# Optimization experiments

Hardware: AMD Instinct MI355X
Metric: run time of the kernel (lower is better)

The kernel has to match this reference:

```python
import jax, jax.numpy as jnp
import numpy as np

D_IN = 1024
D_OUT = 1024
N_HEADS = 16
HEAD_DIM = D_OUT // N_HEADS


def setup_inputs() -> dict:
    key = jax.random.key(0)
    ks = jax.random.split(key, 5)
    scale = 0.02
    x = jax.random.normal(ks[0], (2, 2048, D_IN), dtype=jnp.float32)
    Wq = jax.random.normal(ks[1], (D_IN, D_OUT), dtype=jnp.float32) * scale
    Wk = jax.random.normal(ks[2], (D_IN, D_OUT), dtype=jnp.float32) * scale
    Wv = jax.random.normal(ks[3], (D_IN, D_OUT), dtype=jnp.float32) * scale
    Wout = jax.random.normal(ks[4], (D_OUT, D_OUT), dtype=jnp.float32) * scale
    return {"x": x, "Wq": Wq, "Wk": Wk, "Wv": Wv, "Wout": Wout}


def reference(x, Wq, Wk, Wv, Wout):
    batch, seq_len, _ = x.shape
    # projections (no bias)
    Q = (x @ Wq).reshape(batch, seq_len, N_HEADS, HEAD_DIM)
    K = (x @ Wk).reshape(batch, seq_len, N_HEADS, HEAD_DIM)
    V = (x @ Wv).reshape(batch, seq_len, N_HEADS, HEAD_DIM)
    # scores: [batch, heads, seq, seq]
    scores = jnp.einsum("bqhd,bkhd->bhqk", Q, K) / jnp.sqrt(
        jnp.asarray(HEAD_DIM, dtype=x.dtype)
    )
    # causal mask: positions k > q masked to -inf
    causal = jnp.tril(jnp.ones((seq_len, seq_len), dtype=bool))
    scores = jnp.where(causal[None, None], scores, -jnp.inf)
    weights = jax.nn.softmax(scores, axis=-1)
    vectors = jnp.einsum("bhqk,bkhd->bqhd", weights, V)
    vectors = vectors.reshape(batch, seq_len, D_OUT)
    return vectors @ Wout
```

## Files before the change

### kernel.cpp

```cpp
#include <hip/hip_runtime.h>
#include <hip/hip_bf16.h>


typedef __attribute__((ext_vector_type(8))) _Float16 vhalf8;
typedef __attribute__((ext_vector_type(4))) _Float16 vhalf4;
typedef __attribute__((ext_vector_type(4))) float vfloat4;

#define D_MODEL 1024
#define SEQ     2048
#define NB      2
#define NH      16
#define HD      64

#define SCALE_K1 0.18033688f

__device__ __forceinline__ void async16(const void* g, void* l) {
  __builtin_amdgcn_global_load_lds(
      (const __attribute__((address_space(1))) unsigned int*)g,
      (__attribute__((address_space(3))) unsigned int*)l, 16, 0, 0);
}

__global__ __launch_bounds__(256) void prep(
    const float* __restrict__ x,
    const float* __restrict__ Wq, const float* __restrict__ Wk,
    const float* __restrict__ Wv, const float* __restrict__ Wo,
    _Float16* __restrict__ Xh, _Float16* __restrict__ Wt_qkv,
    _Float16* __restrict__ Wot) {
  int z = blockIdx.z;
  int t = threadIdx.x;
  if (z == 4) {
    int id = blockIdx.y * 16 + blockIdx.x;
#pragma unroll
    for (int pass = 0; pass < 8; pass++) {
      size_t i = ((size_t)(pass * 256 + id) * 256 + t) * 8;
      float4 a = *(const float4*)&x[i];
      float4 b = *(const float4*)&x[i + 4];
      vhalf8 h;
      h[0] = (_Float16)a.x; h[1] = (_Float16)a.y;
      h[2] = (_Float16)a.z; h[3] = (_Float16)a.w;
      h[4] = (_Float16)b.x; h[5] = (_Float16)b.y;
      h[6] = (_Float16)b.z; h[7] = (_Float16)b.w;
      *(vhalf8*)&Xh[i] = h;
    }
    return;
  }
  __shared__ _Float16 tile[64][65];
  const float* in = (z == 0) ? Wq : (z == 1) ? Wk : (z == 2) ? Wv : Wo;
  _Float16* out = (z < 3) ? (Wt_qkv + (size_t)z * 1024 * 1024) : Wot;
  int c0 = blockIdx.x * 64, r0 = blockIdx.y * 64;
  int tc = t & 63, tr = t >> 6;
#pragma unroll
  for (int p = 0; p < 16; p++) {
    int r = tr + p * 4;
    tile[r][tc] = (_Float16)in[(size_t)(r0 + r) * 1024 + c0 + tc];
  }
  __syncthreads();
#pragma unroll
  for (int p = 0; p < 16; p++) {
    int r = tr + p * 4;
    out[(size_t)(c0 + r) * 1024 + r0 + tc] = tile[tc][r];
  }
}

template <int BN>
__global__ __launch_bounds__(256) void gemm128(
    const _Float16* __restrict__ A, const _Float16* __restrict__ Bt,
    _Float16* __restrict__ Ch, float* __restrict__ Cf,
    _Float16* __restrict__ Vt, int M, int N, int K, int mode) {
  constexpr int ACH = 8;
  constexpr int BCH = BN / 16;
  constexpr int CPW = (ACH + BCH) / 4;
  constexpr int JN = BN / 32;
  __shared__ _Float16 As[128 * 32];
  __shared__ _Float16 Bs[BN * 32];
  int m0 = blockIdx.x * 128, n0 = blockIdx.y * BN;
  int t = threadIdx.x;
  int lane = t & 63, wave = t >> 6;
  int wm = (wave >> 1) * 64, wn = (wave & 1) * (BN / 2);
  int col = lane & 15, quad = lane >> 4;
  int srow = lane >> 2;
  int gcol = (((lane & 3) ^ (srow & 3)) << 3);

  vfloat4 acc[4][JN];
#pragma unroll
  for (int i = 0; i < 4; i++)
#pragma unroll
    for (int j = 0; j < JN; j++) {
      acc[i][j][0] = 0.f; acc[i][j][1] = 0.f;
      acc[i][j][2] = 0.f; acc[i][j][3] = 0.f;
    }

  int xq = (quad ^ (col & 3)) * 8;

  for (int k0 = 0; k0 < K; k0 += 32) {
    __syncthreads();
#pragma unroll
    for (int j = 0; j < CPW; j++) {
      int c = wave * CPW + j;
      if (c < ACH) {
        int row = c * 16 + srow;
        async16(&A[(size_t)(m0 + row) * K + k0 + gcol], &As[c * 512]);
      } else {
        int row = (c - ACH) * 16 + srow;
        async16(&Bt[(size_t)(n0 + row) * K + k0 + gcol], &Bs[(c - ACH) * 512]);
      }
    }
    __syncthreads();

    vhalf8 af[4], bf[JN];
#pragma unroll
    for (int i = 0; i < 4; i++)
      af[i] = *(const vhalf8*)&As[(wm + i * 16 + col) * 32 + xq];
#pragma unroll
    for (int j = 0; j < JN; j++)
      bf[j] = *(const vhalf8*)&Bs[(wn + j * 16 + col) * 32 + xq];
#pragma unroll
    for (int i = 0; i < 4; i++)
#pragma unroll
      for (int j = 0; j < JN; j++)
        acc[i][j] = __builtin_amdgcn_mfma_f32_16x16x32_f16(af[i], bf[j], acc[i][j], 0, 0, 0);
  }

  bool vmode = (mode == 2) && (n0 >= 2048);
#pragma unroll
  for (int i = 0; i < 4; i++)
#pragma unroll
    for (int j = 0; j < JN; j++)
#pragma unroll
      for (int r = 0; r < 4; r++) {
        int m = m0 + wm + i * 16 + quad * 4 + r;
        int n = n0 + wn + j * 16 + col;
        if (mode == 1) {
          Cf[(size_t)m * N + n] = acc[i][j][r];
        } else if (vmode) {
          int nn = n - 2048;
          int hh = nn >> 6, dd = nn & 63;
          int bb = m >> 11, ss = m & 2047;
          Vt[(((size_t)bb * NH + hh) * HD + dd) * SEQ + ss] = (_Float16)acc[i][j][r];
        } else {
          Ch[(size_t)m * N + n] = (_Float16)acc[i][j][r];
        }
      }
}

__global__ __launch_bounds__(256) void attn(
    const _Float16* __restrict__ QKV, const _Float16* __restrict__ Vt,
    _Float16* __restrict__ Vec) {
  int blk = blockIdx.x;
  int pp = blk >> 5;
  int hb = blk & 31;
  int h = hb & 15;
  int b = hb >> 4;

  const _Float16* Qb  = QKV + (size_t)(b * SEQ) * 3072 + h * HD;
  const _Float16* Kb  = QKV + (size_t)(b * SEQ) * 3072 + 1024 + h * HD;
  const _Float16* Vtb = Vt + (size_t)(b * NH + h) * HD * SEQ;

  int t = threadIdx.x;
  int lane = t & 63, wave = t >> 6;
  int col = lane & 15, quad = lane >> 4;

  __shared__ _Float16 Ks[64][72];
  __shared__ _Float16 Vs[64][72];
  __shared__ _Float16 Ps[4][16][72];

  int srow = t >> 2;
  int scol = (t & 3) * 16;
  int kslot = ((srow & 3) << 4) + (srow >> 2);
  int kcol = scol ^ ((srow & 3) << 4);

  int tiles[2] = {31 - pp, pp};

  vhalf8 kr0, kr1, vr0, vr1;
  {
    const _Float16* kg = &Kb[(size_t)srow * 3072 + scol];
    kr0 = *(const vhalf8*)kg; kr1 = *(const vhalf8*)(kg + 8);
    const _Float16* vg = &Vtb[(size_t)srow * SEQ + scol];
    vr0 = *(const vhalf8*)vg; vr1 = *(const vhalf8*)(vg + 8);
  }

#pragma unroll
  for (int phase = 0; phase < 2; phase++) {
    int q0 = tiles[phase] * 64;
    int wq0 = q0 + wave * 16;

    vhalf8 qf0 = *(const vhalf8*)&Qb[(size_t)(wq0 + col) * 3072 + quad * 8];
    vhalf8 qf1 = *(const vhalf8*)&Qb[(size_t)(wq0 + col) * 3072 + 32 + quad * 8];
#pragma unroll
    for (int i = 0; i < 8; i++) {
      qf0[i] = qf0[i] * (_Float16)SCALE_K1;
      qf1[i] = qf1[i] * (_Float16)SCALE_K1;
    }

    vfloat4 o[4];
#pragma unroll
    for (int i = 0; i < 4; i++) { o[i][0]=0.f; o[i][1]=0.f; o[i][2]=0.f; o[i][3]=0.f; }
    float lsum[4] = {0.f, 0.f, 0.f, 0.f};

    for (int kb = 0; kb <= q0; kb += 64) {
      *(vhalf8*)&Ks[kslot][kcol]     = kr0;
      *(vhalf8*)&Ks[kslot][kcol + 8] = kr1;
      *(vhalf8*)&Vs[srow][scol]      = vr0;
      *(vhalf8*)&Vs[srow][scol + 8]  = vr1;
      __syncthreads();

      int nxt = (kb < q0) ? (kb + 64) : ((phase == 0) ? 0 : -1);
      if (nxt >= 0) {
        const _Float16* kg = &Kb[(size_t)(nxt + srow) * 3072 + scol];
        kr0 = *(const vhalf8*)kg; kr1 = *(const vhalf8*)(kg + 8);
        const _Float16* vg = &Vtb[(size_t)srow * SEQ + nxt + scol];
        vr0 = *(const vhalf8*)vg; vr1 = *(const vhalf8*)(vg + 8);
      }

      vhalf8 kf[4][2];
#pragma unroll
      for (int hh = 0; hh < 4; hh++) {
        int sw = hh << 4;
        kf[hh][0] = *(const vhalf8*)&Ks[hh * 16 + col][(quad * 8) ^ sw];
        kf[hh][1] = *(const vhalf8*)&Ks[hh * 16 + col][(32 + quad * 8) ^ sw];
      }
      vfloat4 s[4];
#pragma unroll
      for (int hh = 0; hh < 4; hh++) {
        vfloat4 z; z[0]=0.f; z[1]=0.f; z[2]=0.f; z[3]=0.f;
        z = __builtin_amdgcn_mfma_f32_16x16x32_f16(qf0, kf[hh][0], z, 0, 0, 0);
        z = __builtin_amdgcn_mfma_f32_16x16x32_f16(qf1, kf[hh][1], z, 0, 0, 0);
        s[hh] = z;
      }
      bool diag = (kb + 63 > wq0);
#pragma unroll
      for (int r = 0; r < 4; r++) {
        int q = wq0 + quad * 4 + r;
        float p[4];
#pragma unroll
        for (int hh = 0; hh < 4; hh++) {
          float sc = s[hh][r];
          if (diag && (kb + 4 * col + hh > q)) sc = -1e30f;
          p[hh] = __builtin_exp2f(sc);
        }
        lsum[r] += (p[0] + p[1]) + (p[2] + p[3]);
        vhalf4 ph;
        ph[0] = (_Float16)p[0]; ph[1] = (_Float16)p[1];
        ph[2] = (_Float16)p[2]; ph[3] = (_Float16)p[3];
        *(vhalf4*)&Ps[wave][quad * 4 + r][4 * col] = ph;
      }
      __asm__ __volatile__("s_waitcnt lgkmcnt(0)" ::: "memory");
      vhalf8 pf0 = *(const vhalf8*)&Ps[wave][col][quad * 8];
      vhalf8 pf1 = *(const vhalf8*)&Ps[wave][col][32 + quad * 8];
#pragma unroll
      for (int tt = 0; tt < 4; tt++) {
        vhalf8 vf0 = *(const vhalf8*)&Vs[tt * 16 + col][quad * 8];
        vhalf8 vf1 = *(const vhalf8*)&Vs[tt * 16 + col][32 + quad * 8];
        o[tt] = __builtin_amdgcn_mfma_f32_16x16x32_f16(pf0, vf0, o[tt], 0, 0, 0);
        o[tt] = __builtin_amdgcn_mfma_f32_16x16x32_f16(pf1, vf1, o[tt], 0, 0, 0);
      }
      __syncthreads();
    }

    float inv_l[4];
#pragma unroll
    for (int r = 0; r < 4; r++) {
      float rs = lsum[r];
#pragma unroll
      for (int msk = 1; msk < 16; msk <<= 1) rs += __shfl_xor(rs, msk, 64);
      inv_l[r] = 1.0f / rs;
    }
#pragma unroll
    for (int tt = 0; tt < 4; tt++)
#pragma unroll
      for (int r = 0; r < 4; r++) {
        int q = wq0 + quad * 4 + r;
        int d = tt * 16 + col;
        Vec[(size_t)(b * SEQ + q) * D_MODEL + h * HD + d] =
            (_Float16)(o[tt][r] * inv_l[r]);
      }
  }
}

extern "C" void kernel_launch(void* const* d_in, const int* in_sizes, int n_in,
                              void* d_out, int out_size, void* d_ws, size_t ws_size,
                              hipStream_t stream) {
  const float* x  = (const float*)d_in[0];
  const float* Wq = (const float*)d_in[1];
  const float* Wk = (const float*)d_in[2];
  const float* Wv = (const float*)d_in[3];
  const float* Wo = (const float*)d_in[4];
  float* out = (float*)d_out;

  char* ws = (char*)d_ws;
  _Float16* Xh     = (_Float16*)ws;
  _Float16* Wt_qkv = (_Float16*)(ws + 8388608);
  _Float16* Wot    = (_Float16*)(ws + 14680064);
  _Float16* QKV    = (_Float16*)(ws + 16777216);
  _Float16* Vt     = (_Float16*)(ws + 41943040);
  _Float16* Vec    = (_Float16*)(ws + 50331648);

  dim3 tb(256);
  prep<<<dim3(16, 16, 5), tb, 0, stream>>>(x, Wq, Wk, Wv, Wo, Xh, Wt_qkv, Wot);
  gemm128<128><<<dim3(32, 24), tb, 0, stream>>>(Xh, Wt_qkv, QKV, nullptr, Vt,
                                                4096, 3072, 1024, 2);
  attn<<<dim3(512), tb, 0, stream>>>(QKV, Vt, Vec);
  gemm128<64><<<dim3(32, 16), tb, 0, stream>>>(Vec, Wot, nullptr, out, nullptr,
                                               4096, 1024, 1024, 1);
}
```

Baseline: 192.7 us.

## Split attention KV loop across two wave groups and vectorize V-transpose stores

The attention kernel now runs 512 threads per block. Two groups of four waves each process alternating 64-wide key tiles with separate K/V LDS buffers, and their partial outputs and row sums are merged through shared memory at the end. This doubles per-block parallelism over the causal key loop, which was previously serial per block, at the cost of more LDS, an extra reduction step and a barrier. Separately, the V-transpose epilogue of the QKV GEMM packs four consecutive sequence values into one 8-byte store instead of four scalar stores.

```diff
diff --git a/kernel.cpp b/kernel.cpp
--- a/kernel.cpp
+++ b/kernel.cpp
@@ -125,25 +125,32 @@
 #pragma unroll
   for (int i = 0; i < 4; i++)
 #pragma unroll
-    for (int j = 0; j < JN; j++)
-#pragma unroll
-      for (int r = 0; r < 4; r++) {
-        int m = m0 + wm + i * 16 + quad * 4 + r;
+    for (int j = 0; j < JN; j++) {
+      if (vmode) {
         int n = n0 + wn + j * 16 + col;
-        if (mode == 1) {
-          Cf[(size_t)m * N + n] = acc[i][j][r];
-        } else if (vmode) {
-          int nn = n - 2048;
-          int hh = nn >> 6, dd = nn & 63;
-          int bb = m >> 11, ss = m & 2047;
-          Vt[(((size_t)bb * NH + hh) * HD + dd) * SEQ + ss] = (_Float16)acc[i][j][r];
-        } else {
-          Ch[(size_t)m * N + n] = (_Float16)acc[i][j][r];
-        }
-      }
-}
-
-__global__ __launch_bounds__(256) void attn(
+        int nn = n - 2048;
+        int hh = nn >> 6, dd = nn & 63;
+        int m_base = m0 + wm + i * 16 + quad * 4;
+        int bb = m_base >> 11, ss = m_base & 2047;
+        vhalf4 pk;
+        pk[0] = (_Float16)acc[i][j][0]; pk[1] = (_Float16)acc[i][j][1];
+        pk[2] = (_Float16)acc[i][j][2]; pk[3] = (_Float16)acc[i][j][3];
+        *(vhalf4*)&Vt[(((size_t)bb * NH + hh) * HD + dd) * SEQ + ss] = pk;
+      } else {
+#pragma unroll
+        for (int r = 0; r < 4; r++) {
+          int m = m0 + wm + i * 16 + quad * 4 + r;
+          int n = n0 + wn + j * 16 + col;
+          if (mode == 1)
+            Cf[(size_t)m * N + n] = acc[i][j][r];
+          else
+            Ch[(size_t)m * N + n] = (_Float16)acc[i][j][r];
+        }
+      }
+    }
+}
+
+__global__ __launch_bounds__(512) void attn(
     const _Float16* __restrict__ QKV, const _Float16* __restrict__ Vt,
     _Float16* __restrict__ Vec) {
   int blk = blockIdx.x;
@@ -158,14 +165,18 @@
 
   int t = threadIdx.x;
   int lane = t & 63, wave = t >> 6;
+  int sw = wave & 3, hf = wave >> 2;
   int col = lane & 15, quad = lane >> 4;
 
-  __shared__ _Float16 Ks[64][72];
-  __shared__ _Float16 Vs[64][72];
-  __shared__ _Float16 Ps[4][16][72];
-
-  int srow = t >> 2;
-  int scol = (t & 3) * 16;
+  __shared__ _Float16 Ks[2][64][72];
+  __shared__ _Float16 Vs[2][64][72];
+  __shared__ _Float16 Ps[8][16][72];
+  __shared__ float Om[64][65];
+  __shared__ float Lm[64];
+
+  int tl = t & 255;
+  int srow = tl >> 2;
+  int scol = (tl & 3) * 16;
   int kslot = ((srow & 3) << 4) + (srow >> 2);
   int kcol = scol ^ ((srow & 3) << 4);
 
@@ -173,16 +184,19 @@
 
   vhalf8 kr0, kr1, vr0, vr1;
   {
-    const _Float16* kg = &Kb[(size_t)srow * 3072 + scol];
+    const _Float16* kg = &Kb[(size_t)(hf * 64 + srow) * 3072 + scol];
     kr0 = *(const vhalf8*)kg; kr1 = *(const vhalf8*)(kg + 8);
-    const _Float16* vg = &Vtb[(size_t)srow * SEQ + scol];
+    const _Float16* vg = &Vtb[(size_t)srow * SEQ + hf * 64 + scol];
     vr0 = *(const vhalf8*)vg; vr1 = *(const vhalf8*)(vg + 8);
   }
 
 #pragma unroll
   for (int phase = 0; phase < 2; phase++) {
-    int q0 = tiles[phase] * 64;
-    int wq0 = q0 + wave * 16;
+    int qt = tiles[phase];
+    int q0 = qt * 64;
+    int ntk = qt + 1;
+    int J = (ntk + 1) >> 1;
+    int wq0 = q0 + sw * 16;
 
     vhalf8 qf0 = *(const vhalf8*)&Qb[(size_t)(wq0 + col) * 3072 + quad * 8];
     vhalf8 qf1 = *(const vhalf8*)&Qb[(size_t)(wq0 + col) * 3072 + 32 + quad * 8];
@@ -197,83 +211,114 @@
     for (int i = 0; i < 4; i++) { o[i][0]=0.f; o[i][1]=0.f; o[i][2]=0.f; o[i][3]=0.f; }
     float lsum[4] = {0.f, 0.f, 0.f, 0.f};
 
-    for (int kb = 0; kb <= q0; kb += 64) {
-      *(vhalf8*)&Ks[kslot][kcol]     = kr0;
-      *(vhalf8*)&Ks[kslot][kcol + 8] = kr1;
-      *(vhalf8*)&Vs[srow][scol]      = vr0;
-      *(vhalf8*)&Vs[srow][scol + 8]  = vr1;
+    for (int j = 0; j < J; j++) {
+      int ti = 2 * j + hf;
+      bool active = (ti < ntk);
+      int kb = ti * 64;
+      if (active) {
+        *(vhalf8*)&Ks[hf][kslot][kcol]     = kr0;
+        *(vhalf8*)&Ks[hf][kslot][kcol + 8] = kr1;
+        *(vhalf8*)&Vs[hf][srow][scol]      = vr0;
+        *(vhalf8*)&Vs[hf][srow][scol + 8]  = vr1;
+      }
       __syncthreads();
 
-      int nxt = (kb < q0) ? (kb + 64) : ((phase == 0) ? 0 : -1);
-      if (nxt >= 0) {
-        const _Float16* kg = &Kb[(size_t)(nxt + srow) * 3072 + scol];
+      {
+        int tnext;
+        if (phase == 0)
+          tnext = (ti + 2 < ntk) ? (ti + 2) : hf;
+        else
+          tnext = (ti + 2 < ntk) ? (ti + 2) : ti;
+        int kpf = tnext * 64;
+        const _Float16* kg = &Kb[(size_t)(kpf + srow) * 3072 + scol];
         kr0 = *(const vhalf8*)kg; kr1 = *(const vhalf8*)(kg + 8);
-        const _Float16* vg = &Vtb[(size_t)srow * SEQ + nxt + scol];
+        const _Float16* vg = &Vtb[(size_t)srow * SEQ + kpf + scol];
         vr0 = *(const vhalf8*)vg; vr1 = *(const vhalf8*)(vg + 8);
       }
 
-      vhalf8 kf[4][2];
-#pragma unroll
-      for (int hh = 0; hh < 4; hh++) {
-        int sw = hh << 4;
-        kf[hh][0] = *(const vhalf8*)&Ks[hh * 16 + col][(quad * 8) ^ sw];
-        kf[hh][1] = *(const vhalf8*)&Ks[hh * 16 + col][(32 + quad * 8) ^ sw];
-      }
-      vfloat4 s[4];
-#pragma unroll
-      for (int hh = 0; hh < 4; hh++) {
-        vfloat4 z; z[0]=0.f; z[1]=0.f; z[2]=0.f; z[3]=0.f;
-        z = __builtin_amdgcn_mfma_f32_16x16x32_f16(qf0, kf[hh][0], z, 0, 0, 0);
-        z = __builtin_amdgcn_mfma_f32_16x16x32_f16(qf1, kf[hh][1], z, 0, 0, 0);
-        s[hh] = z;
-      }
-      bool diag = (kb + 63 > wq0);
-#pragma unroll
-      for (int r = 0; r < 4; r++) {
-        int q = wq0 + quad * 4 + r;
-        float p[4];
+      if (active) {
+        vhalf8 kf[4][2];
 #pragma unroll
         for (int hh = 0; hh < 4; hh++) {
-          float sc = s[hh][r];
-          if (diag && (kb + 4 * col + hh > q)) sc = -1e30f;
-          p[hh] = __builtin_exp2f(sc);
-        }
-        lsum[r] += (p[0] + p[1]) + (p[2] + p[3]);
-        vhalf4 ph;
-        ph[0] = (_Float16)p[0]; ph[1] = (_Float16)p[1];
-        ph[2] = (_Float16)p[2]; ph[3] = (_Float16)p[3];
-        *(vhalf4*)&Ps[wave][quad * 4 + r][4 * col] = ph;
-      }
-      __asm__ __volatile__("s_waitcnt lgkmcnt(0)" ::: "memory");
-      vhalf8 pf0 = *(const vhalf8*)&Ps[wave][col][quad * 8];
-      vhalf8 pf1 = *(const vhalf8*)&Ps[wave][col][32 + quad * 8];
-#pragma unroll
-      for (int tt = 0; tt < 4; tt++) {
-        vhalf8 vf0 = *(const vhalf8*)&Vs[tt * 16 + col][quad * 8];
-        vhalf8 vf1 = *(const vhalf8*)&Vs[tt * 16 + col][32 + quad * 8];
-        o[tt] = __builtin_amdgcn_mfma_f32_16x16x32_f16(pf0, vf0, o[tt], 0, 0, 0);
-        o[tt] = __builtin_amdgcn_mfma_f32_16x16x32_f16(pf1, vf1, o[tt], 0, 0, 0);
+          int swz = hh << 4;
+          kf[hh][0] = *(const vhalf8*)&Ks[hf][hh * 16 + col][(quad * 8) ^ swz];
+          kf[hh][1] = *(const vhalf8*)&Ks[hf][hh * 16 + col][(32 + quad * 8) ^ swz];
+        }
+        vfloat4 s[4];
+#pragma unroll
+        for (int hh = 0; hh < 4; hh++) {
+          vfloat4 z; z[0]=0.f; z[1]=0.f; z[2]=0.f; z[3]=0.f;
+          z = __builtin_amdgcn_mfma_f32_16x16x32_f16(qf0, kf[hh][0], z, 0, 0, 0);
+          z = __builtin_amdgcn_mfma_f32_16x16x32_f16(qf1, kf[hh][1], z, 0, 0, 0);
+          s[hh] = z;
+        }
+        bool diag = (kb + 63 > wq0);
+#pragma unroll
+        for (int r = 0; r < 4; r++) {
+          int q = wq0 + quad * 4 + r;
+          float p[4];
+#pragma unroll
+          for (int hh = 0; hh < 4; hh++) {
+            float sc = s[hh][r];
+            if (diag && (kb + 4 * col + hh > q)) sc = -1e30f;
+            p[hh] = __builtin_exp2f(sc);
+          }
+          lsum[r] += (p[0] + p[1]) + (p[2] + p[3]);
+          vhalf4 ph;
+          ph[0] = (_Float16)p[0]; ph[1] = (_Float16)p[1];
+          ph[2] = (_Float16)p[2]; ph[3] = (_Float16)p[3];
+          *(vhalf4*)&Ps[wave][quad * 4 + r][4 * col] = ph;
+        }
+        __asm__ __volatile__("s_waitcnt lgkmcnt(0)" ::: "memory");
+        vhalf8 pf0 = *(const vhalf8*)&Ps[wave][col][quad * 8];
+        vhalf8 pf1 = *(const vhalf8*)&Ps[wave][col][32 + quad * 8];
+#pragma unroll
+        for (int tt = 0; tt < 4; tt++) {
+          vhalf8 vf0 = *(const vhalf8*)&Vs[hf][tt * 16 + col][quad * 8];
+          vhalf8 vf1 = *(const vhalf8*)&Vs[hf][tt * 16 + col][32 + quad * 8];
+          o[tt] = __builtin_amdgcn_mfma_f32_16x16x32_f16(pf0, vf0, o[tt], 0, 0, 0);
+          o[tt] = __builtin_amdgcn_mfma_f32_16x16x32_f16(pf1, vf1, o[tt], 0, 0, 0);
+        }
       }
       __syncthreads();
     }
 
-    float inv_l[4];
+    float rs[4];
 #pragma unroll
     for (int r = 0; r < 4; r++) {
-      float rs = lsum[r];
-#pragma unroll
-      for (int msk = 1; msk < 16; msk <<= 1) rs += __shfl_xor(rs, msk, 64);
-      inv_l[r] = 1.0f / rs;
-    }
-#pragma unroll
-    for (int tt = 0; tt < 4; tt++)
-#pragma unroll
-      for (int r = 0; r < 4; r++) {
-        int q = wq0 + quad * 4 + r;
-        int d = tt * 16 + col;
-        Vec[(size_t)(b * SEQ + q) * D_MODEL + h * HD + d] =
-            (_Float16)(o[tt][r] * inv_l[r]);
-      }
+      float v = lsum[r];
+#pragma unroll
+      for (int msk = 1; msk < 16; msk <<= 1) v += __shfl_xor(v, msk, 64);
+      rs[r] = v;
+    }
+    if (hf == 1) {
+#pragma unroll
+      for (int tt = 0; tt < 4; tt++)
+#pragma unroll
+        for (int r = 0; r < 4; r++)
+          Om[sw * 16 + quad * 4 + r][tt * 16 + col] = o[tt][r];
+      if (col == 0)
+#pragma unroll
+        for (int r = 0; r < 4; r++)
+          Lm[sw * 16 + quad * 4 + r] = rs[r];
+    }
+    __syncthreads();
+    if (hf == 0) {
+      float inv_l[4];
+#pragma unroll
+      for (int r = 0; r < 4; r++)
+        inv_l[r] = 1.0f / (rs[r] + Lm[sw * 16 + quad * 4 + r]);
+#pragma unroll
+      for (int tt = 0; tt < 4; tt++)
+#pragma unroll
+        for (int r = 0; r < 4; r++) {
+          int q = wq0 + quad * 4 + r;
+          int d = tt * 16 + col;
+          float ov = o[tt][r] + Om[sw * 16 + quad * 4 + r][tt * 16 + col];
+          Vec[(size_t)(b * SEQ + q) * D_MODEL + h * HD + d] =
+              (_Float16)(ov * inv_l[r]);
+        }
+    }
   }
 }
 
@@ -299,7 +344,7 @@
   prep<<<dim3(16, 16, 5), tb, 0, stream>>>(x, Wq, Wk, Wv, Wo, Xh, Wt_qkv, Wot);
   gemm128<128><<<dim3(32, 24), tb, 0, stream>>>(Xh, Wt_qkv, QKV, nullptr, Vt,
                                                 4096, 3072, 1024, 2);
-  attn<<<dim3(512), tb, 0, stream>>>(QKV, Vt, Vec);
+  attn<<<dim3(512), dim3(512), 0, stream>>>(QKV, Vt, Vec);
   gemm128<64><<<dim3(32, 16), tb, 0, stream>>>(Vec, Wot, nullptr, out, nullptr,
                                                4096, 1024, 1024, 1);
 }
```

After: 184.0 us. -4.5%, faster.
